# Performance work log

Hardware: AMD Instinct MI355X
Metric: run time of the kernel (lower is better)

The kernel has to match this reference:

```python
import jax, jax.numpy as jnp
import numpy as np

B, S, H = 2, 2048, 4096
NH, NKV, HD = 32, 8, 128
EPS = 1e-6


def _rope_tables(seq_len, head_dim, base=10000.0):
    inv = 1.0 / (base ** (np.arange(0, head_dim, 2, dtype=np.float32) / head_dim))
    t = np.arange(seq_len, dtype=np.float32)
    freqs = np.outer(t, inv)                       # [S, HD/2]
    emb = np.concatenate([freqs, freqs], axis=-1)  # [S, HD] (HF rotate_half layout)
    return jnp.asarray(np.cos(emb)), jnp.asarray(np.sin(emb))


def setup_inputs() -> dict:
    key = jax.random.key(0)
    ks = jax.random.split(key, 6)
    x = jax.random.normal(ks[0], (B, S, H), dtype=jnp.float32)
    wq = jax.random.normal(ks[1], (NH * HD, H), dtype=jnp.float32) * 0.02
    wk = jax.random.normal(ks[2], (NKV * HD, H), dtype=jnp.float32) * 0.02
    wv = jax.random.normal(ks[3], (NKV * HD, H), dtype=jnp.float32) * 0.02
    wo = jax.random.normal(ks[4], (H, NH * HD), dtype=jnp.float32) * 0.02
    cos1, sin1 = _rope_tables(S, HD)
    cos = jnp.broadcast_to(cos1[None], (B, S, HD))
    sin = jnp.broadcast_to(sin1[None], (B, S, HD))
    return {
        "x": x, "cos": cos, "sin": sin,
        "wq": wq, "wk": wk, "wv": wv, "wo": wo,
        "q_norm_w": jnp.ones((HD,), jnp.float32),
        "k_norm_w": jnp.ones((HD,), jnp.float32),
    }


def _rms_norm(x, w):
    # fp32 RMSNorm over last dim, scaled by per-head-dim weight
    xf = x.astype(jnp.float32)
    n = xf * jax.lax.rsqrt(jnp.mean(xf * xf, axis=-1, keepdims=True) + EPS)
    return n.astype(x.dtype) * w


def _rotate_half(x):
    x1, x2 = jnp.split(x, 2, axis=-1)
    return jnp.concatenate([-x2, x1], axis=-1)


def reference(x, cos, sin, wq, wk, wv, wo, q_norm_w, k_norm_w):
    bs, seqlen, _ = x.shape
    # projections (nn.Linear: y = x @ W^T)
    xq = (x @ wq.T).reshape(bs, seqlen, NH, HD)
    xk = (x @ wk.T).reshape(bs, seqlen, NKV, HD)
    xv = (x @ wv.T).reshape(bs, seqlen, NKV, HD)
    # per-head RMSNorm before RoPE
    xq = _rms_norm(xq, q_norm_w)
    xk = _rms_norm(xk, k_norm_w)
    # [b, h, s, d]
    xq = xq.transpose(0, 2, 1, 3)
    xk = xk.transpose(0, 2, 1, 3)
    xv = xv.transpose(0, 2, 1, 3)
    # RoPE, cos/sin broadcast over heads
    c = cos[:, None, :, :]
    s = sin[:, None, :, :]
    xq = xq * c + _rotate_half(xq) * s
    xk = xk * c + _rotate_half(xk) * s
    # GQA: repeat kv heads
    rep = NH // NKV
    if rep > 1:
        xk = jnp.repeat(xk, rep, axis=1)
        xv = jnp.repeat(xv, rep, axis=1)
    # causal SDPA
    scale = 1.0 / jnp.sqrt(jnp.float32(HD))
    scores = jnp.einsum("bhqd,bhkd->bhqk", xq, xk) * scale
    mask = jnp.tril(jnp.ones((seqlen, seqlen), bool))
    scores = jnp.where(mask, scores, jnp.finfo(scores.dtype).min)
    probs = jax.nn.softmax(scores, axis=-1)
    out = jnp.einsum("bhqk,bhkd->bhqd", probs, xv)
    out = out.transpose(0, 2, 1, 3).reshape(bs, seqlen, NH * HD)
    return out @ wo.T
```

## Files before the change

### kernel.cpp

```cpp
#include <hip/hip_runtime.h>
#include <hip/hip_bf16.h>

#define NB  2
#define SS  2048
#define HH  4096
#define NH  32
#define NKV 8
#define HD  128
#define MR  (NB*SS)

typedef __bf16 bf16x8 __attribute__((ext_vector_type(8)));
typedef float  f32x4  __attribute__((ext_vector_type(4)));
typedef float  f32x16 __attribute__((ext_vector_type(16)));
using bf16 = __hip_bfloat16;

__device__ __forceinline__ f32x4 mfma16(bf16x8 a, bf16x8 b, f32x4 c) {
  return __builtin_amdgcn_mfma_f32_16x16x32_bf16(a, b, c, 0, 0, 0);
}
__device__ __forceinline__ f32x16 mfma32(bf16x8 a, bf16x8 b, f32x16 c) {
  return __builtin_amdgcn_mfma_f32_32x32x16_bf16(a, b, c, 0, 0, 0);
}
__device__ __forceinline__ unsigned cvtpk(float lo, float hi) {
  unsigned r; asm("v_cvt_pk_bf16_f32 %0, %1, %2" : "=v"(r) : "v"(lo), "v"(hi));
  return r;
}
__device__ __forceinline__ void swap32(unsigned &a, unsigned &b) {
  asm volatile("v_permlane32_swap_b32 %0, %1" : "+v"(a), "+v"(b));
}
__device__ __forceinline__ float fexp2(float x) {
  float r; asm("v_exp_f32 %0, %1" : "=v"(r) : "v"(x)); return r;
}

typedef const __attribute__((address_space(1))) void gv_t;
typedef __attribute__((address_space(3))) void lv_t;
__device__ __forceinline__ void gload16(const void* g, void* l) {
  __builtin_amdgcn_global_load_lds((gv_t*)g, (lv_t*)l, 16, 0, 0);
}
#define CFENCE asm volatile("" ::: "memory")

__global__ void f2b5(const float* __restrict__ s0, const float* __restrict__ s1,
                     const float* __restrict__ s2, const float* __restrict__ s3,
                     const float* __restrict__ s4,
                     bf16* __restrict__ d0, bf16* __restrict__ d1,
                     bf16* __restrict__ d2, bf16* __restrict__ d3,
                     bf16* __restrict__ d4)
{
  const unsigned c0 = 4194304u, c1 = 8388608u, c2 = 9437184u, c3 = 10485760u,
                 c4 = 14680064u;
  unsigned i = blockIdx.x*blockDim.x + threadIdx.x;
  unsigned stride = gridDim.x*blockDim.x;
  for (unsigned u = i; u < c4; u += stride) {
    const float* s; bf16* d; unsigned off;
    if (u < c0)      { s = s0; d = d0; off = u; }
    else if (u < c1) { s = s1; d = d1; off = u - c0; }
    else if (u < c2) { s = s2; d = d2; off = u - c1; }
    else if (u < c3) { s = s3; d = d3; off = u - c2; }
    else             { s = s4; d = d4; off = u - c3; }
    float4 v = *(const float4*)(s + (size_t)off*4);
    __hip_bfloat16 b0 = __float2bfloat16(v.x);
    __hip_bfloat16 b1 = __float2bfloat16(v.y);
    __hip_bfloat16 b2 = __float2bfloat16(v.z);
    __hip_bfloat16 b3 = __float2bfloat16(v.w);
    ushort4 o;
    o.x = *reinterpret_cast<unsigned short*>(&b0);
    o.y = *reinterpret_cast<unsigned short*>(&b1);
    o.z = *reinterpret_cast<unsigned short*>(&b2);
    o.w = *reinterpret_cast<unsigned short*>(&b3);
    *(ushort4*)((unsigned short*)d + (size_t)off*4) = o;
  }
}

template<typename OutT>
__global__ __launch_bounds__(512, 2) void gemm256(
    const bf16* __restrict__ A, const bf16* __restrict__ Bt, OutT* __restrict__ C,
    int M, int N, int K, int tilesX)
{
  __shared__ bf16 lds[2*2*2*8192];

  const int bid = blockIdx.x;
  const int cpx = gridDim.x >> 3;
  const int wg  = (bid & 7)*cpx + (bid >> 3);
  const int m0 = (wg / tilesX) * 256, n0 = (wg % tilesX) * 256;

  const int tid = threadIdx.x;
  const int l = tid & 63;
  const int l15 = l & 15, lhi = l >> 4;
  const int wid = tid >> 6;
  const int wr = wid >> 2, wc = wid & 3;

  const int srow = tid >> 2;
  const int sps  = tid & 3;
  const int sls  = (sps - (srow >> 1)) & 3;
  const bf16* ga0 = A  + (size_t)(m0 + srow)*K       + sls*8;
  const bf16* ga1 = A  + (size_t)(m0 + srow + 128)*K + sls*8;
  const bf16* gb0 = Bt + (size_t)(n0 + srow)*K       + sls*8;
  const bf16* gb1 = Bt + (size_t)(n0 + srow + 128)*K + sls*8;
  const int ldst = tid*8;

#define REG(buf, mat, ks) (&lds[(((buf)*2 + (mat))*2 + (ks))*8192])
#define STG_A(buf, ks, kofs) do {                                 \
    gload16(ga0 + (kofs), REG(buf,0,ks) + ldst);                  \
    gload16(ga1 + (kofs), REG(buf,0,ks) + ldst + 4096);           \
  } while (0)
#define STG_B(buf, ks, kofs) do {                                 \
    gload16(gb0 + (kofs), REG(buf,1,ks) + ldst);                  \
    gload16(gb1 + (kofs), REG(buf,1,ks) + ldst + 4096);           \
  } while (0)

  f32x4 acc[8][4];
  #pragma unroll
  for (int fm = 0; fm < 8; ++fm)
    #pragma unroll
    for (int fn = 0; fn < 4; ++fn)
      #pragma unroll
      for (int e = 0; e < 4; ++e) acc[fm][fn][e] = 0.f;

  const int arow = wr*128 + l15;
  const int brow = wc*64  + l15;
  const int psl  = (lhi + (l15 >> 1)) & 3;

  bf16x8 bv[4];

#define PHASE(PB, KS, FMH, RB, STG, WN) do {                               \
    const bf16* Ar_ = REG(PB, 0, KS);                                      \
    const bf16* Br_ = REG(PB, 1, KS);                                      \
    bf16x8 af[4];                                                          \
    for (int fm = 0; fm < 4; ++fm)                                         \
      af[fm] = *(const bf16x8*)(Ar_ + (arow + (FMH)*64 + fm*16)*32 + psl*8); \
    if (RB) {                                                              \
      for (int fn = 0; fn < 4; ++fn)                                       \
        bv[fn] = *(const bf16x8*)(Br_ + (brow + fn*16)*32 + psl*8);        \
    }                                                                      \
    STG;                                                                   \
    CFENCE;                                                                \
    __builtin_amdgcn_s_barrier();                                          \
    __builtin_amdgcn_s_setprio(1);                                         \
    for (int fm = 0; fm < 4; ++fm)                                         \
      for (int fn = 0; fn < 4; ++fn)                                       \
        acc[(FMH)*4 + fm][fn] = mfma16(af[fm], bv[fn], acc[(FMH)*4 + fm][fn]); \
    __builtin_amdgcn_s_setprio(0);                                         \
    if ((WN) == 6)      asm volatile("s_waitcnt vmcnt(6)" ::: "memory");   \
    else if ((WN) == 0) asm volatile("s_waitcnt vmcnt(0)" ::: "memory");   \
    __builtin_amdgcn_s_barrier();                                          \
    CFENCE;                                                                \
  } while (0)

  const int nt = K >> 6;

  STG_A(0, 0, 0);  STG_B(0, 0, 0);  STG_A(0, 1, 32);  STG_B(0, 1, 32);
  STG_A(1, 0, 64); STG_B(1, 0, 64); STG_B(1, 1, 96);
  asm volatile("s_waitcnt vmcnt(6)" ::: "memory");
  __builtin_amdgcn_s_barrier();
  CFENCE;

  for (int i = 0; i < (nt >> 1) - 1; ++i) {
    const int t  = i << 1;
    const int k1 = ((t + 1) << 6) + 32;
    const int k2 = (t + 2) << 6;
    const int k3 = (t + 3) << 6;
    PHASE(0, 0, 0, true,  STG_A(1, 1, k1),      -1);
    PHASE(0, 0, 1, false, STG_B(0, 0, k2),      -1);
    PHASE(0, 1, 0, true,  STG_A(0, 0, k2),      -1);
    PHASE(0, 1, 1, false, STG_B(0, 1, k2 + 32),  6);
    PHASE(1, 0, 0, true,  STG_A(0, 1, k2 + 32), -1);
    PHASE(1, 0, 1, false, STG_B(1, 0, k3),      -1);
    PHASE(1, 1, 0, true,  STG_A(1, 0, k3),      -1);
    PHASE(1, 1, 1, false, STG_B(1, 1, k3 + 32),  6);
  }
  {
    const int k1 = ((nt - 1) << 6) + 32;
    PHASE(0, 0, 0, true,  STG_A(1, 1, k1), -1);
    PHASE(0, 0, 1, false, (void)0,         -1);
    PHASE(0, 1, 0, true,  (void)0,         -1);
    PHASE(0, 1, 1, false, (void)0,          0);
    PHASE(1, 0, 0, true,  (void)0,         -1);
    PHASE(1, 0, 1, false, (void)0,         -1);
    PHASE(1, 1, 0, true,  (void)0,         -1);
    PHASE(1, 1, 1, false, (void)0,         -1);
  }
#undef PHASE
#undef STG_A
#undef STG_B
#undef REG

  #pragma unroll
  for (int fm = 0; fm < 8; ++fm) {
    const int crow = m0 + wr*128 + fm*16 + lhi*4;
    #pragma unroll
    for (int fn = 0; fn < 4; ++fn) {
      const int ccol = n0 + wc*64 + fn*16 + l15;
      #pragma unroll
      for (int j = 0; j < 4; ++j) {
        if constexpr (sizeof(OutT) == 2)
          C[(size_t)(crow + j)*N + ccol] = __float2bfloat16(acc[fm][fn][j]);
        else
          C[(size_t)(crow + j)*N + ccol] = acc[fm][fn][j];
      }
    }
  }
}

__global__ __launch_bounds__(512, 2) void gemm128n(
    const bf16* __restrict__ A, const bf16* __restrict__ Bt, bf16* __restrict__ C,
    int M, int N, int K, int tilesX)
{
  __shared__ bf16 lds[2*2*12288];

  const int bid = blockIdx.x;
  const int cpx = gridDim.x >> 3;
  const int wg  = (bid & 7)*cpx + (bid >> 3);
  const int m0 = (wg / tilesX) * 128, n0 = (wg % tilesX) * 256;

  const int tid = threadIdx.x;
  const int l = tid & 63;
  const int l15 = l & 15, lhi = l >> 4;
  const int wid = tid >> 6;
  const int wr = wid >> 2, wc = wid & 3;

  const int srow = tid >> 2;
  const int sps  = tid & 3;
  const int sls  = (sps - (srow >> 1)) & 3;
  const bf16* gaA = A  + (size_t)(m0 + srow)*K       + sls*8;
  const bf16* gb0 = Bt + (size_t)(n0 + srow)*K       + sls*8;
  const bf16* gb1 = Bt + (size_t)(n0 + srow + 128)*K + sls*8;
  const int ldst = tid*8;

#define REGA(buf, ks) (&lds[((buf)*2 + (ks))*12288])
#define REGB(buf, ks) (&lds[((buf)*2 + (ks))*12288 + 4096])
#define STGKA(buf, ks, kofs) gload16(gaA + (kofs), REGA(buf,ks) + ldst)
#define STGKB(buf, ks, kofs) do {                                 \
    gload16(gb0 + (kofs), REGB(buf,ks) + ldst);                   \
    gload16(gb1 + (kofs), REGB(buf,ks) + ldst + 4096);            \
  } while (0)

  f32x4 acc[4][4];
  #pragma unroll
  for (int fm = 0; fm < 4; ++fm)
    #pragma unroll
    for (int fn = 0; fn < 4; ++fn)
      #pragma unroll
      for (int e = 0; e < 4; ++e) acc[fm][fn][e] = 0.f;

  const int arow = wr*64 + l15;
  const int brow = wc*64 + l15;
  const int psl  = (lhi + (l15 >> 1)) & 3;

#define PHASEK(PB, KS, STG, WN) do {                                       \
    const bf16* Ar_ = REGA(PB, KS);                                        \
    const bf16* Br_ = REGB(PB, KS);                                        \
    bf16x8 af[4], bv[4];                                                   \
    for (int fm = 0; fm < 4; ++fm)                                         \
      af[fm] = *(const bf16x8*)(Ar_ + (arow + fm*16)*32 + psl*8);          \
    for (int fn = 0; fn < 4; ++fn)                                         \
      bv[fn] = *(const bf16x8*)(Br_ + (brow + fn*16)*32 + psl*8);          \
    STG;                                                                   \
    CFENCE;                                                                \
    __builtin_amdgcn_s_barrier();                                          \
    __builtin_amdgcn_s_setprio(1);                                         \
    for (int fm = 0; fm < 4; ++fm)                                         \
      for (int fn = 0; fn < 4; ++fn)                                       \
        acc[fm][fn] = mfma16(af[fm], bv[fn], acc[fm][fn]);                 \
    __builtin_amdgcn_s_setprio(0);                                         \
    if ((WN) == 6)      asm volatile("s_waitcnt vmcnt(6)" ::: "memory");   \
    else if ((WN) == 0) asm volatile("s_waitcnt vmcnt(0)" ::: "memory");   \
    __builtin_amdgcn_s_barrier();                                          \
    CFENCE;                                                                \
  } while (0)

  const int nt = K >> 6;

  STGKB(0, 0, 0);  STGKA(0, 0, 0);  STGKB(0, 1, 32);  STGKA(0, 1, 32);
  STGKB(1, 0, 64); STGKA(1, 0, 64); STGKB(1, 1, 96);  STGKA(1, 1, 96);
  asm volatile("s_waitcnt vmcnt(6)" ::: "memory");
  __builtin_amdgcn_s_barrier();
  CFENCE;

  for (int i = 0; i < (nt >> 1) - 1; ++i) {
    const int t  = i << 1;
    const int k2 = (t + 2) << 6;
    const int k3 = (t + 3) << 6;
    PHASEK(0, 0, { STGKB(0, 0, k2);      STGKA(0, 0, k2);      }, -1);
    PHASEK(0, 1, { STGKB(0, 1, k2 + 32); STGKA(0, 1, k2 + 32); },  6);
    PHASEK(1, 0, { STGKB(1, 0, k3);      STGKA(1, 0, k3);      }, -1);
    PHASEK(1, 1, { STGKB(1, 1, k3 + 32); STGKA(1, 1, k3 + 32); },  6);
  }
  {
    PHASEK(0, 0, (void)0, -1);
    PHASEK(0, 1, (void)0,  0);
    PHASEK(1, 0, (void)0, -1);
    PHASEK(1, 1, (void)0, -1);
  }
#undef PHASEK
#undef STGKA
#undef STGKB
#undef REGA
#undef REGB

  #pragma unroll
  for (int fm = 0; fm < 4; ++fm) {
    const int crow = m0 + wr*64 + fm*16 + lhi*4;
    #pragma unroll
    for (int fn = 0; fn < 4; ++fn) {
      const int ccol = n0 + wc*64 + fn*16 + l15;
      #pragma unroll
      for (int j = 0; j < 4; ++j)
        C[(size_t)(crow + j)*N + ccol] = __float2bfloat16(acc[fm][fn][j]);
    }
  }
}

__global__ __launch_bounds__(256) void normrope(
    const bf16* __restrict__ src, bf16* __restrict__ dst,
    const float* __restrict__ cosb, const float* __restrict__ sinb,
    const float* __restrict__ w, int nh, float scale, int rowstride, int coloff)
{
  const int wid = threadIdx.x >> 6, lane = threadIdx.x & 63;
  const int row = blockIdx.x*4 + wid;
  const int m = row / nh, h = row % nh;
  const int b = m / SS, s = m % SS;
  const bf16* sp = src + (size_t)m*rowstride + coloff + h*HD;
  float v1 = __bfloat162float(sp[lane]);
  float v2 = __bfloat162float(sp[lane + 64]);
  float ss = v1*v1 + v2*v2;
  #pragma unroll
  for (int msk = 1; msk < 64; msk <<= 1) ss += __shfl_xor(ss, msk);
  float r = rsqrtf(ss*(1.f/128.f) + 1e-6f) * scale;
  float n1 = v1*r*w[lane], n2 = v2*r*w[lane + 64];
  const float* cp  = cosb + (size_t)m*HD;
  const float* sip = sinb + (size_t)m*HD;
  float o1 = n1*cp[lane]      - n2*sip[lane];
  float o2 = n2*cp[lane + 64] + n1*sip[lane + 64];
  bf16* dp = dst + ((size_t)(b*nh + h)*SS + s)*HD;
  dp[lane]      = __float2bfloat16(o1);
  dp[lane + 64] = __float2bfloat16(o2);
}

__global__ __launch_bounds__(256) void vtrans(const bf16* __restrict__ v0,
                                              bf16* __restrict__ vt,
                                              int rowstride, int coloff)
{
  __shared__ bf16 tile[64][65];
  const int s0 = blockIdx.x*64, d0 = blockIdx.y*64, bkv = blockIdx.z;
  const int bb = bkv >> 3, kv = bkv & 7;
  const int c = threadIdx.x & 63, rbase = threadIdx.x >> 6;
  #pragma unroll
  for (int r = 0; r < 64; r += 4) {
    int sl = r + rbase;
    tile[sl][c] = v0[(size_t)(bb*SS + s0 + sl)*rowstride + coloff + kv*HD + d0 + c];
  }
  __syncthreads();
  #pragma unroll
  for (int r = 0; r < 64; r += 4) {
    int dl = r + rbase;
    vt[((size_t)bkv*HD + d0 + dl)*SS + s0 + c] = tile[c][dl];
  }
}

__global__ __launch_bounds__(512, 2) void attn_fwd(
    const bf16* __restrict__ qr, const bf16* __restrict__ kr,
    const bf16* __restrict__ vt, bf16* __restrict__ ao)
{
  __shared__ __align__(16) char smem[65536];

  const int L = blockIdx.x;
  const int orig = (L & 7)*64 + (L >> 3);
  const int bh = orig >> 3, j = orig & 7;
  const int b = bh >> 5, h = bh & 31, kvh = h >> 2;

  const int tid = threadIdx.x;
  const int wid = tid >> 6, lane = tid & 63;
  const int l31 = lane & 31, hi = lane >> 5;
  const unsigned hi16 = hi << 4;
  const unsigned swz = (lane & 7) << 4;

  const int qw0 = (wid < 4) ? (j*128 + wid*32) : ((15 - j)*128 + (wid - 4)*32);
  const int NT = 32 - 2*j;
  const int qlane = qw0 + l31;

  const bf16* Qp = qr + ((size_t)(b*NH + h)*SS + qlane)*HD;
  const bf16* Kp = kr + (size_t)(b*NKV + kvh)*SS*HD;
  const bf16* Vp = vt + (size_t)(b*NKV + kvh)*HD*SS;

  const int krA = tid >> 4;
  const int ksA = tid & 15;
  const int vrA = tid >> 3;
  const int vsA = tid & 7;
  const int kswz = (ksA ^ (krA & 7))*8;
  const int vswz = (vsA ^ (vrA & 7))*8;

#define STAGE_ATTN(buf, kvbase) do {                                        \
    char* kb = smem + (buf)*32768;                                          \
    char* vb = kb + 16384;                                                  \
    gload16(Kp + (size_t)(krA + (kvbase))*HD + kswz,      kb + tid*16);     \
    gload16(Kp + (size_t)(krA + 32 + (kvbase))*HD + kswz, kb + 8192 + tid*16); \
    gload16(Vp + (size_t)vrA*SS + (kvbase) + vswz,        vb + tid*16);     \
    gload16(Vp + (size_t)(vrA + 64)*SS + (kvbase) + vswz, vb + 8192 + tid*16); \
  } while (0)

  STAGE_ATTN(0, 0);
  bf16x8 qf[8];
  #pragma unroll
  for (int kd = 0; kd < 8; ++kd)
    qf[kd] = *(const bf16x8*)(Qp + kd*16 + hi*8);
  asm volatile("s_waitcnt vmcnt(0)" ::: "memory");
  __builtin_amdgcn_s_barrier();
  CFENCE;

  f32x16 o0, o1, o2, o3;
  #pragma unroll
  for (int r = 0; r < 16; ++r) { o0[r] = 0.f; o1[r] = 0.f; o2[r] = 0.f; o3[r] = 0.f; }
  float mrow = -1e30f, lrow = 0.f;

  for (int t = 0; t < NT; ++t) {
    const int p = t & 1;
    const char* KsB = smem + p*32768;
    const char* VsB = KsB + 16384;
    if (t + 1 < NT) STAGE_ATTN(p ^ 1, (t + 1)*64);
    const int kv0 = t*64;

    if (kv0 <= qw0 + 31) {
      f32x16 s0, s1;
      #pragma unroll
      for (int r = 0; r < 16; ++r) { s0[r] = 0.f; s1[r] = 0.f; }
      #pragma unroll
      for (int kd = 0; kd < 8; ++kd) {
        bf16x8 k0f = *(const bf16x8*)(KsB + l31*256        + (((unsigned)(kd*32) + hi16) ^ swz));
        bf16x8 k1f = *(const bf16x8*)(KsB + (32 + l31)*256 + (((unsigned)(kd*32) + hi16) ^ swz));
        s0 = mfma32(k0f, qf[kd], s0);
        s1 = mfma32(k1f, qf[kd], s1);
      }
      if (kv0 + 63 > qw0) {
        #pragma unroll
        for (int r = 0; r < 16; ++r) {
          const int off = (r & 3) + 8*(r >> 2) + 4*hi;
          if (kv0 + off > qlane)      s0[r] = -1e30f;
          if (kv0 + 32 + off > qlane) s1[r] = -1e30f;
        }
      }
      float tmax = s0[0];
      #pragma unroll
      for (int r = 1; r < 16; ++r) tmax = fmaxf(tmax, s0[r]);
      #pragma unroll
      for (int r = 0; r < 16; ++r) tmax = fmaxf(tmax, s1[r]);
      tmax = fmaxf(tmax, __shfl_xor(tmax, 32));
      if (!__all(tmax <= mrow + 8.f)) {
        float mnew = fmaxf(mrow, tmax);
        float alpha = fexp2(mrow - mnew);
        mrow = mnew;
        lrow *= alpha;
        #pragma unroll
        for (int r = 0; r < 16; ++r) {
          o0[r] *= alpha; o1[r] *= alpha; o2[r] *= alpha; o3[r] *= alpha;
        }
      }
      float tsum = 0.f;
      #pragma unroll
      for (int r = 0; r < 16; ++r) { s0[r] = fexp2(s0[r] - mrow); tsum += s0[r]; }
      #pragma unroll
      for (int r = 0; r < 16; ++r) { s1[r] = fexp2(s1[r] - mrow); tsum += s1[r]; }
      tsum += __shfl_xor(tsum, 32);
      lrow += tsum;

      #pragma unroll
      for (int ks = 0; ks < 4; ++ks) {
        const int bb0 = (ks & 1)*8;
        float p0,p1,p2,p3,p4,p5,p6,p7;
        if (ks < 2) { p0=s0[bb0+0];p1=s0[bb0+1];p2=s0[bb0+2];p3=s0[bb0+3];
                      p4=s0[bb0+4];p5=s0[bb0+5];p6=s0[bb0+6];p7=s0[bb0+7]; }
        else        { p0=s1[bb0+0];p1=s1[bb0+1];p2=s1[bb0+2];p3=s1[bb0+3];
                      p4=s1[bb0+4];p5=s1[bb0+5];p6=s1[bb0+6];p7=s1[bb0+7]; }
        unsigned c01 = cvtpk(p0,p1), c23 = cvtpk(p2,p3);
        unsigned c45 = cvtpk(p4,p5), c67 = cvtpk(p6,p7);
        unsigned w0 = c01, w2 = c45; swap32(w0, w2);
        unsigned w1 = c23, w3 = c67; swap32(w1, w3);
        union { unsigned u[4]; bf16x8 v; } pa;
        pa.u[0]=w0; pa.u[1]=w1; pa.u[2]=w2; pa.u[3]=w3;
        #pragma unroll
        for (int dt = 0; dt < 4; ++dt) {
          bf16x8 vf = *(const bf16x8*)(VsB + (dt*32 + l31)*128 +
                                       (((unsigned)(ks*32) + hi16) ^ swz));
          f32x16 &oo = (dt==0)?o0:(dt==1)?o1:(dt==2)?o2:o3;
          oo = mfma32(vf, pa.v, oo);
        }
      }
    }

    asm volatile("s_waitcnt vmcnt(0)" ::: "memory");
    __builtin_amdgcn_s_barrier();
    CFENCE;
  }
#undef STAGE_ATTN

  const float invl = 1.f / lrow;
  char* ow = smem + wid*4096;
  bf16* aop = ao + ((size_t)b*SS + qlane)*HH + h*HD;
  const unsigned eswz = (l31 & 7) << 4;
  #pragma unroll
  for (int half = 0; half < 2; ++half) {
    #pragma unroll
    for (int hh = 0; hh < 2; ++hh) {
      #pragma unroll
      for (int r = 0; r < 16; ++r) {
        const int dcol = hh*32 + (r & 3) + 8*(r >> 2) + 4*hi;
        float val = ((half*2+hh)==0 ? o0[r] : (half*2+hh)==1 ? o1[r]
                     : (half*2+hh)==2 ? o2[r] : o3[r]) * invl;
        *(bf16*)(ow + l31*128 + (((unsigned)(dcol*2)) ^ eswz)) = __float2bfloat16(val);
      }
    }
    #pragma unroll
    for (int m = 0; m < 4; ++m) {
      const int c0 = hi*32 + m*8;
      bf16x8 vv = *(const bf16x8*)(ow + l31*128 + (((unsigned)(c0*2)) ^ eswz));
      *(bf16x8*)(aop + half*64 + c0) = vv;
    }
  }
}

extern "C" void kernel_launch(void* const* d_in, const int* in_sizes, int n_in,
                              void* d_out, int out_size, void* d_ws, size_t ws_size,
                              hipStream_t stream)
{
  const float* x    = (const float*)d_in[0];
  const float* cosb = (const float*)d_in[1];
  const float* sinb = (const float*)d_in[2];
  const float* wq   = (const float*)d_in[3];
  const float* wk   = (const float*)d_in[4];
  const float* wv   = (const float*)d_in[5];
  const float* wo   = (const float*)d_in[6];
  const float* qnw  = (const float*)d_in[7];
  const float* knw  = (const float*)d_in[8];
  float* out = (float*)d_out;

  char* ws = (char*)d_ws;
  bf16* xb    = (bf16*)(ws);
  bf16* wqkvb = (bf16*)(ws +  33554432);
  bf16* wob   = (bf16*)(ws +  83886080);
  bf16* q0    = (bf16*)(ws + 117440512);
  bf16* kv0   = (bf16*)(ws + 150994944);
  bf16* qr    = (bf16*)(ws + 167772160);
  bf16* vt = xb;
  bf16* kr = (bf16*)(ws + 8388608);
  bf16* ao = q0;

  f2b5<<<2048, 256, 0, stream>>>(x, wq, wk, wv, wo,
                                 xb, wqkvb,
                                 wqkvb + (size_t)4096*4096,
                                 wqkvb + (size_t)5120*4096,
                                 wob);

  gemm256<bf16><<<256, 512, 0, stream>>>(xb, wqkvb, q0, MR, 4096, HH, 16);
  gemm128n<<<256, 512, 0, stream>>>(xb, wqkvb + (size_t)4096*4096, kv0,
                                    MR, 2048, HH, 8);

  normrope<<<(MR*NH)/4,  256, 0, stream>>>(q0, qr, cosb, sinb, qnw, NH,
                                           0.08838834764831845f*1.44269504088896341f,
                                           4096, 0);
  normrope<<<(MR*NKV)/4, 256, 0, stream>>>(kv0, kr, cosb, sinb, knw, NKV, 1.0f,
                                           2048, 0);
  vtrans<<<dim3(32, 2, 16), 256, 0, stream>>>(kv0, vt, 2048, 1024);

  attn_fwd<<<512, 512, 0, stream>>>(qr, kr, vt, ao);

  gemm256<float><<<256, 512, 0, stream>>>(ao, wob, out, MR, HH, HH, 16);
}
```

Before: 517.4 us.

## Merge GEMM phases into full-tile steps and add MFMA priority in attention

```diff
diff --git a/kernel.cpp b/kernel.cpp
--- a/kernel.cpp
+++ b/kernel.cpp
@@ -119,27 +119,24 @@
   const int brow = wc*64  + l15;
   const int psl  = (lhi + (l15 >> 1)) & 3;
 
-  bf16x8 bv[4];
-
-#define PHASE(PB, KS, FMH, RB, STG, WN) do {                               \
+#define PHASE(PB, KS, STG, WN) do {                                        \
     const bf16* Ar_ = REG(PB, 0, KS);                                      \
     const bf16* Br_ = REG(PB, 1, KS);                                      \
-    bf16x8 af[4];                                                          \
-    for (int fm = 0; fm < 4; ++fm)                                         \
-      af[fm] = *(const bf16x8*)(Ar_ + (arow + (FMH)*64 + fm*16)*32 + psl*8); \
-    if (RB) {                                                              \
-      for (int fn = 0; fn < 4; ++fn)                                       \
-        bv[fn] = *(const bf16x8*)(Br_ + (brow + fn*16)*32 + psl*8);        \
-    }                                                                      \
+    bf16x8 af[8], bv[4];                                                   \
+    for (int fm = 0; fm < 8; ++fm)                                         \
+      af[fm] = *(const bf16x8*)(Ar_ + (arow + fm*16)*32 + psl*8);          \
+    for (int fn = 0; fn < 4; ++fn)                                         \
+      bv[fn] = *(const bf16x8*)(Br_ + (brow + fn*16)*32 + psl*8);          \
     STG;                                                                   \
     CFENCE;                                                                \
     __builtin_amdgcn_s_barrier();                                          \
     __builtin_amdgcn_s_setprio(1);                                         \
-    for (int fm = 0; fm < 4; ++fm)                                         \
+    for (int fm = 0; fm < 8; ++fm)                                         \
       for (int fn = 0; fn < 4; ++fn)                                       \
-        acc[(FMH)*4 + fm][fn] = mfma16(af[fm], bv[fn], acc[(FMH)*4 + fm][fn]); \
+        acc[fm][fn] = mfma16(af[fm], bv[fn], acc[fm][fn]);                 \
     __builtin_amdgcn_s_setprio(0);                                         \
-    if ((WN) == 6)      asm volatile("s_waitcnt vmcnt(6)" ::: "memory");   \
+    if ((WN) == 8)      asm volatile("s_waitcnt vmcnt(8)" ::: "memory");   \
+    else if ((WN) == 4) asm volatile("s_waitcnt vmcnt(4)" ::: "memory");   \
     else if ((WN) == 0) asm volatile("s_waitcnt vmcnt(0)" ::: "memory");   \
     __builtin_amdgcn_s_barrier();                                          \
     CFENCE;                                                                \
@@ -147,9 +144,10 @@
 
   const int nt = K >> 6;
 
-  STG_A(0, 0, 0);  STG_B(0, 0, 0);  STG_A(0, 1, 32);  STG_B(0, 1, 32);
-  STG_A(1, 0, 64); STG_B(1, 0, 64); STG_B(1, 1, 96);
-  asm volatile("s_waitcnt vmcnt(6)" ::: "memory");
+  STG_A(0, 0, 0);  STG_B(0, 0, 0);
+  STG_A(0, 1, 32); STG_B(0, 1, 32);
+  STG_A(1, 0, 64); STG_B(1, 0, 64);
+  asm volatile("s_waitcnt vmcnt(8)" ::: "memory");
   __builtin_amdgcn_s_barrier();
   CFENCE;
 
@@ -158,25 +156,17 @@
     const int k1 = ((t + 1) << 6) + 32;
     const int k2 = (t + 2) << 6;
     const int k3 = (t + 3) << 6;
-    PHASE(0, 0, 0, true,  STG_A(1, 1, k1),      -1);
-    PHASE(0, 0, 1, false, STG_B(0, 0, k2),      -1);
-    PHASE(0, 1, 0, true,  STG_A(0, 0, k2),      -1);
-    PHASE(0, 1, 1, false, STG_B(0, 1, k2 + 32),  6);
-    PHASE(1, 0, 0, true,  STG_A(0, 1, k2 + 32), -1);
-    PHASE(1, 0, 1, false, STG_B(1, 0, k3),      -1);
-    PHASE(1, 1, 0, true,  STG_A(1, 0, k3),      -1);
-    PHASE(1, 1, 1, false, STG_B(1, 1, k3 + 32),  6);
+    PHASE(0, 0, { STG_A(1, 1, k1);      STG_B(1, 1, k1);      }, 8);
+    PHASE(0, 1, { STG_A(0, 0, k2);      STG_B(0, 0, k2);      }, 8);
+    PHASE(1, 0, { STG_A(0, 1, k2 + 32); STG_B(0, 1, k2 + 32); }, 8);
+    PHASE(1, 1, { STG_A(1, 0, k3);      STG_B(1, 0, k3);      }, 8);
   }
   {
     const int k1 = ((nt - 1) << 6) + 32;
-    PHASE(0, 0, 0, true,  STG_A(1, 1, k1), -1);
-    PHASE(0, 0, 1, false, (void)0,         -1);
-    PHASE(0, 1, 0, true,  (void)0,         -1);
-    PHASE(0, 1, 1, false, (void)0,          0);
-    PHASE(1, 0, 0, true,  (void)0,         -1);
-    PHASE(1, 0, 1, false, (void)0,         -1);
-    PHASE(1, 1, 0, true,  (void)0,         -1);
-    PHASE(1, 1, 1, false, (void)0,         -1);
+    PHASE(0, 0, { STG_A(1, 1, k1); STG_B(1, 1, k1); }, 8);
+    PHASE(0, 1, (void)0,  4);
+    PHASE(1, 0, (void)0,  0);
+    PHASE(1, 1, (void)0, -1);
   }
 #undef PHASE
 #undef STG_A
@@ -422,6 +412,7 @@
       f32x16 s0, s1;
       #pragma unroll
       for (int r = 0; r < 16; ++r) { s0[r] = 0.f; s1[r] = 0.f; }
+      __builtin_amdgcn_s_setprio(1);
       #pragma unroll
       for (int kd = 0; kd < 8; ++kd) {
         bf16x8 k0f = *(const bf16x8*)(KsB + l31*256        + (((unsigned)(kd*32) + hi16) ^ swz));
@@ -429,6 +420,7 @@
         s0 = mfma32(k0f, qf[kd], s0);
         s1 = mfma32(k1f, qf[kd], s1);
       }
+      __builtin_amdgcn_s_setprio(0);
       if (kv0 + 63 > qw0) {
         #pragma unroll
         for (int r = 0; r < 16; ++r) {
@@ -437,11 +429,13 @@
           if (kv0 + 32 + off > qlane) s1[r] = -1e30f;
         }
       }
-      float tmax = s0[0];
-      #pragma unroll
-      for (int r = 1; r < 16; ++r) tmax = fmaxf(tmax, s0[r]);
-      #pragma unroll
-      for (int r = 0; r < 16; ++r) tmax = fmaxf(tmax, s1[r]);
+      float mg[8];
+      #pragma unroll
+      for (int r = 0; r < 8; ++r)
+        mg[r] = fmaxf(fmaxf(s0[r], s0[r + 8]), fmaxf(s1[r], s1[r + 8]));
+      float ta = fmaxf(fmaxf(mg[0], mg[1]), mg[2]);
+      float tb = fmaxf(fmaxf(mg[3], mg[4]), mg[5]);
+      float tmax = fmaxf(fmaxf(ta, tb), fmaxf(mg[6], mg[7]));
       tmax = fmaxf(tmax, __shfl_xor(tmax, 32));
       if (!__all(tmax <= mrow + 8.f)) {
         float mnew = fmaxf(mrow, tmax);
@@ -475,6 +469,7 @@
         unsigned w1 = c23, w3 = c67; swap32(w1, w3);
         union { unsigned u[4]; bf16x8 v; } pa;
         pa.u[0]=w0; pa.u[1]=w1; pa.u[2]=w2; pa.u[3]=w3;
+        __builtin_amdgcn_s_setprio(1);
         #pragma unroll
         for (int dt = 0; dt < 4; ++dt) {
           bf16x8 vf = *(const bf16x8*)(VsB + (dt*32 + l31)*128 +
@@ -482,6 +477,7 @@
           f32x16 &oo = (dt==0)?o0:(dt==1)?o1:(dt==2)?o2:o3;
           oo = mfma32(vf, pa.v, oo);
         }
+        __builtin_amdgcn_s_setprio(0);
       }
     }
 
```

Measured after the change: 535.9 us. 1.04x slower.
